# Optimization experiments

Hardware: AMD Instinct MI355X
Metric: run time of the kernel (lower is better)

Reference implementation:

```python
import jax, jax.numpy as jnp
import numpy as np

H = 512      # hidden_channels
NP = 20000   # politician nodes
NS = 10000   # stock nodes
E = 400000   # edges per relation / trade edges
FP = 64      # raw politician feature dim
FS = 64      # raw stock feature dim
NC = 3       # num_classes


def setup_inputs() -> dict:
    key = jax.random.key(0)
    ks = iter(jax.random.split(key, 40))

    def rn(shape, s=0.05):
        return (jax.random.normal(next(ks), shape, jnp.float32) * s).astype(jnp.float32)

    inp = {}
    inp["x_pol"] = rn((NP, FP), 1.0)
    inp["x_stock"] = rn((NS, FS), 1.0)
    inp["trade_edge_attr"] = rn((E, 2), 1.0)
    # input projections (torch Linear: y = x @ W + b)
    inp["Wp"] = rn((FP, H)); inp["bp"] = rn((H,))
    inp["Ws"] = rn((FS, H)); inp["bs"] = rn((H,))
    # SAGEConv params: Wl/bl act on mean-aggregated neighbors, Wr on root (no bias)
    for layer in ("c1", "c2"):
        for rel in ("ps", "sp"):
            inp[f"{layer}_{rel}_Wl"] = rn((H, H))
            inp[f"{layer}_{rel}_bl"] = rn((H,))
            inp[f"{layer}_{rel}_Wr"] = rn((H, H))
    # decoder MLP
    inp["d1_W"] = rn((2 * H + 2, H)); inp["d1_b"] = rn((H,))
    inp["d2_W"] = rn((H, NC)); inp["d2_b"] = rn((NC,))
    # edge indices
    inp["edge_ps_src"] = jax.random.randint(next(ks), (E,), 0, NP, jnp.int64 if jax.config.jax_enable_x64 else jnp.int32)
    inp["edge_ps_dst"] = jax.random.randint(next(ks), (E,), 0, NS, jnp.int32)
    inp["edge_sp_src"] = jax.random.randint(next(ks), (E,), 0, NS, jnp.int32)
    inp["edge_sp_dst"] = jax.random.randint(next(ks), (E,), 0, NP, jnp.int32)
    inp["trade_row"] = jax.random.randint(next(ks), (E,), 0, NP, jnp.int32)
    inp["trade_col"] = jax.random.randint(next(ks), (E,), 0, NS, jnp.int32)
    inp["edge_ps_src"] = inp["edge_ps_src"].astype(jnp.int32)
    return inp


def sage_conv(x_src, x_dst, src, dst, Wl, bl, Wr, n_dst):
    # PyG SAGEConv (aggr='mean', root_weight=True, normalize=False):
    # out = lin_l(mean_{j->i} x_j) + lin_r(x_i)
    msg = x_src[src]                                            # [E, H] gather
    agg = jax.ops.segment_sum(msg, dst, num_segments=n_dst)     # [n_dst, H]
    cnt = jax.ops.segment_sum(jnp.ones((src.shape[0], 1), x_src.dtype), dst, num_segments=n_dst)
    mean = agg / jnp.maximum(cnt, 1.0)
    return mean @ Wl + bl + x_dst @ Wr


def reference(x_pol, x_stock, trade_edge_attr,
              Wp, bp, Ws, bs,
              c1_ps_Wl, c1_ps_bl, c1_ps_Wr, c1_sp_Wl, c1_sp_bl, c1_sp_Wr,
              c2_ps_Wl, c2_ps_bl, c2_ps_Wr, c2_sp_Wl, c2_sp_bl, c2_sp_Wr,
              d1_W, d1_b, d2_W, d2_b,
              edge_ps_src, edge_ps_dst, edge_sp_src, edge_sp_dst,
              trade_row, trade_col):
    # per-node-type input projection + relu
    hp = jax.nn.relu(x_pol @ Wp + bp)      # [NP, H]
    hs = jax.nn.relu(x_stock @ Ws + bs)    # [NS, H]
    # conv1 (HeteroConv sum: each node type is dst of exactly one relation)
    hs1 = sage_conv(hp, hs, edge_ps_src, edge_ps_dst, c1_ps_Wl, c1_ps_bl, c1_ps_Wr, hs.shape[0])
    hp1 = sage_conv(hs, hp, edge_sp_src, edge_sp_dst, c1_sp_Wl, c1_sp_bl, c1_sp_Wr, hp.shape[0])
    hp1, hs1 = jax.nn.relu(hp1), jax.nn.relu(hs1)
    # conv2
    hs2 = sage_conv(hp1, hs1, edge_ps_src, edge_ps_dst, c2_ps_Wl, c2_ps_bl, c2_ps_Wr, hs1.shape[0])
    hp2 = sage_conv(hs1, hp1, edge_sp_src, edge_sp_dst, c2_sp_Wl, c2_sp_bl, c2_sp_Wr, hp1.shape[0])
    hp2, hs2 = jax.nn.relu(hp2), jax.nn.relu(hs2)
    # edge decoder (Dropout is identity at inference)
    feat = jnp.concatenate([hp2[trade_row], hs2[trade_col], trade_edge_attr], axis=-1)  # [E, 2H+2]
    h = jax.nn.relu(feat @ d1_W + d1_b)
    return h @ d2_W + d2_b  # [E, NC]
```

## Files before the change

kernel.cpp:

```cpp
#include <hip/hip_runtime.h>
#include <hip/hip_bf16.h>

typedef unsigned short u16;
typedef unsigned int u32;
typedef __attribute__((ext_vector_type(8))) short short8;
typedef __attribute__((ext_vector_type(4))) float f32x4;

#define NP 20000
#define NS 10000
#define NE 400000
#define H  512
#define FDIM 64
#define ECHUNK 16

__device__ __forceinline__ float bl16(u32 w){ return __uint_as_float(w << 16); }
__device__ __forceinline__ float bh16(u32 w){ return __uint_as_float(w & 0xffff0000u); }
__device__ __forceinline__ u16 f2bf(float f){
  u32 u = __float_as_uint(f);
  u32 r = u + 0x7fffu + ((u >> 16) & 1u);
  return (u16)(r >> 16);
}
__device__ __forceinline__ u32 pack2(float a, float b){
  return (u32)f2bf(a) | ((u32)f2bf(b) << 16);
}
__device__ __forceinline__ void gload16(const void* g, void* l){
  __builtin_amdgcn_global_load_lds((const __attribute__((address_space(1))) u32*)g,
                                   (__attribute__((address_space(3))) u32*)l, 16, 0, 0);
}

__global__ __launch_bounds__(256) void proj_kernel(const float* __restrict__ X, const float* __restrict__ W,
                                                   const float* __restrict__ b, u16* __restrict__ Y, int n)
{
  __shared__ float xs[8][FDIM];
  int tid = threadIdx.x;
  int m0 = blockIdx.x * 8;
  {
    int r = tid >> 6, c = tid & 63;
    int m = m0 + r;
    xs[r][c] = (m < n) ? X[(size_t)m*FDIM + c] : 0.f;
    m = m0 + r + 4;
    xs[r+4][c] = (m < n) ? X[(size_t)m*FDIM + c] : 0.f;
  }
  __syncthreads();
  float acc[8][2] = {};
  int c0 = tid, c1 = tid + 256;
  for (int k = 0; k < FDIM; ++k){
    float w0 = W[k*H + c0];
    float w1 = W[k*H + c1];
    #pragma unroll
    for (int r = 0; r < 8; ++r){
      float xv = xs[r][k];
      acc[r][0] = fmaf(xv, w0, acc[r][0]);
      acc[r][1] = fmaf(xv, w1, acc[r][1]);
    }
  }
  float b0 = b[c0], b1 = b[c1];
  #pragma unroll
  for (int r = 0; r < 8; ++r){
    int m = m0 + r;
    if (m < n){
      Y[(size_t)m*H + c0] = f2bf(fmaxf(acc[r][0] + b0, 0.f));
      Y[(size_t)m*H + c1] = f2bf(fmaxf(acc[r][1] + b1, 0.f));
    }
  }
}

struct TPair { const float* src; u16* dst; };
struct TArgs { TPair m[10]; };

__global__ __launch_bounds__(256) void wtrans_kernel(TArgs args)
{
  __shared__ float lds[32][33];
  int mat = blockIdx.z;
  const float* __restrict__ src = args.m[mat].src;
  u16* __restrict__ dst = args.m[mat].dst;
  int k0 = blockIdx.y << 5, n0 = blockIdx.x << 5;
  int t = threadIdx.x;
  int r = t >> 3, c4 = (t & 7) << 2;
  float4 v = *(const float4*)(src + (size_t)(k0 + r)*H + n0 + c4);
  lds[r][c4+0] = v.x; lds[r][c4+1] = v.y; lds[r][c4+2] = v.z; lds[r][c4+3] = v.w;
  __syncthreads();
  uint2 o;
  o.x = pack2(lds[c4+0][r], lds[c4+1][r]);
  o.y = pack2(lds[c4+2][r], lds[c4+3][r]);
  *(uint2*)(dst + (size_t)(n0 + r)*H + k0 + c4) = o;
}

__global__ void hist_kernel(const int* __restrict__ ps_dst, const int* __restrict__ sp_dst,
                            const int* __restrict__ trow,
                            int* __restrict__ cnt_s, int* __restrict__ cnt_p, int* __restrict__ cnt_t)
{
  int e = blockIdx.x * blockDim.x + threadIdx.x;
  if (e < NE){
    atomicAdd(&cnt_s[ps_dst[e]], 1);
    atomicAdd(&cnt_p[sp_dst[e]], 1);
    atomicAdd(&cnt_t[trow[e]], 1);
  }
}

__device__ void scan_one(int* cnt, int n, int* rowptr)
{
  __shared__ int lds[1024];
  __shared__ int carry_s;
  int tid = threadIdx.x;
  if (tid == 0) carry_s = 0;
  __syncthreads();
  for (int base = 0; base < n; base += 1024){
    int i = base + tid;
    int v = (i < n) ? cnt[i] : 0;
    lds[tid] = v;
    __syncthreads();
    for (int off = 1; off < 1024; off <<= 1){
      int t = (tid >= off) ? lds[tid - off] : 0;
      __syncthreads();
      lds[tid] += t;
      __syncthreads();
    }
    int incl = lds[tid];
    int cb = carry_s;
    if (i < n){
      rowptr[i] = cb + incl - v;
      cnt[i] = cb + incl - v;
    }
    __syncthreads();
    if (tid == 0) carry_s = cb + lds[1023];
    __syncthreads();
  }
  if (tid == 0) rowptr[n] = carry_s;
}

__global__ __launch_bounds__(1024) void scan3_kernel(int* c0, int n0, int* r0,
                                                     int* c1, int n1, int* r1,
                                                     int* c2, int n2, int* r2)
{
  if (blockIdx.x == 0) scan_one(c0, n0, r0);
  else if (blockIdx.x == 1) scan_one(c1, n1, r1);
  else scan_one(c2, n2, r2);
}

__global__ void scatter_kernel(const int* __restrict__ ps_src, const int* __restrict__ ps_dst,
                               const int* __restrict__ sp_src, const int* __restrict__ sp_dst,
                               const int* __restrict__ trow, const int* __restrict__ tcol,
                               const float* __restrict__ attr,
                               int* __restrict__ cur_s, int* __restrict__ cur_p, int* __restrict__ cur_t,
                               int* __restrict__ sorted_ps, int* __restrict__ sorted_sp,
                               int4* __restrict__ meta_t, float2* __restrict__ attr_t)
{
  int e = blockIdx.x * blockDim.x + threadIdx.x;
  if (e < NE){
    int pos = atomicAdd(&cur_s[ps_dst[e]], 1);
    sorted_ps[pos] = ps_src[e];
    int pos2 = atomicAdd(&cur_p[sp_dst[e]], 1);
    sorted_sp[pos2] = sp_src[e];
    int r = trow[e];
    int pos3 = atomicAdd(&cur_t[r], 1);
    meta_t[pos3] = make_int4(e, r, tcol[e], 0);
    attr_t[pos3] = make_float2(attr[2*e], attr[2*e+1]);
  }
}

__global__ __launch_bounds__(256) void agg2_kernel(
    const u16* __restrict__ X0, const int* __restrict__ rp0, const int* __restrict__ s0,
    u16* __restrict__ M0, int n0,
    const u16* __restrict__ X1, const int* __restrict__ rp1, const int* __restrict__ s1,
    u16* __restrict__ M1, int n1)
{
  int wid = (blockIdx.x << 2) + (threadIdx.x >> 6);
  int lane = threadIdx.x & 63;
  const u16* X; const int* rp; const int* ss; u16* M; int row;
  if (wid < n0){ X = X0; rp = rp0; ss = s0; M = M0; row = wid; }
  else if (wid < n0 + n1){ X = X1; rp = rp1; ss = s1; M = M1; row = wid - n0; }
  else return;
  int beg = rp[row], end = rp[row + 1];
  float acc[8] = {0,0,0,0,0,0,0,0};
  int j0 = lane << 3;
#define ACCV(v) { acc[0] += bl16(v.x); acc[1] += bh16(v.x); \
                  acc[2] += bl16(v.y); acc[3] += bh16(v.y); \
                  acc[4] += bl16(v.z); acc[5] += bh16(v.z); \
                  acc[6] += bl16(v.w); acc[7] += bh16(v.w); }
  int i = beg;
  for (; i + 4 <= end; i += 4){
    int sa = ss[i], sb = ss[i+1], sc = ss[i+2], sd = ss[i+3];
    uint4 v0 = *(const uint4*)(X + (size_t)sa*H + j0);
    uint4 v1 = *(const uint4*)(X + (size_t)sb*H + j0);
    uint4 v2 = *(const uint4*)(X + (size_t)sc*H + j0);
    uint4 v3 = *(const uint4*)(X + (size_t)sd*H + j0);
    ACCV(v0); ACCV(v1); ACCV(v2); ACCV(v3);
  }
  for (; i < end; ++i){
    int sa = ss[i];
    uint4 v0 = *(const uint4*)(X + (size_t)sa*H + j0);
    ACCV(v0);
  }
#undef ACCV
  float inv = 1.f / (float)max(end - beg, 1);
  uint4 o;
  o.x = pack2(acc[0]*inv, acc[1]*inv);
  o.y = pack2(acc[2]*inv, acc[3]*inv);
  o.z = pack2(acc[4]*inv, acc[5]*inv);
  o.w = pack2(acc[6]*inv, acc[7]*inv);
  *(uint4*)(M + (size_t)row*H + j0) = o;
}

struct GemmProb {
  const u16* A1; const u16* W1t; const u16* A2; const u16* W2t;
  const float* bias; u16* C; int nrows; int relu;
};

__global__ __launch_bounds__(256) void gemm_mfma2(GemmProb Pa, GemmProb Pb)
{
  GemmProb P = blockIdx.z ? Pb : Pa;
  int m0 = blockIdx.y << 7, n0 = blockIdx.x << 7;
  if (m0 >= P.nrows) return;

  __shared__ u16 As[128*64];
  __shared__ u16 Bs[128*64];
  char* AsB = (char*)As;
  char* BsB = (char*)Bs;
  int t = threadIdx.x;
  int w = t >> 6, l = t & 63;
  int wr = w >> 1, wc = w & 1;
  int lr = l & 15, lg = l >> 4;

  f32x4 acc[4][4];
  #pragma unroll
  for (int i = 0; i < 4; ++i)
    #pragma unroll
    for (int j = 0; j < 4; ++j)
      acc[i][j] = (f32x4){0.f, 0.f, 0.f, 0.f};

  for (int phase = 0; phase < 2; ++phase){
    const u16* Ap = phase ? P.A2 : P.A1;
    const u16* Wp = phase ? P.W2t : P.W1t;
    if (!Ap) break;
    for (int k0 = 0; k0 < H; k0 += 64){
      #pragma unroll
      for (int i = 0; i < 4; ++i){
        int c = i*256 + t;
        int row = c >> 3, p = c & 7;
        int k8 = p ^ (row & 7);
        gload16(Ap + (size_t)(m0 + row)*H + k0 + k8*8, AsB + c*16);
        gload16(Wp + (size_t)(n0 + row)*H + k0 + k8*8, BsB + c*16);
      }
      __syncthreads();
      #pragma unroll
      for (int ks = 0; ks < 2; ++ks){
        short8 a[4], b[4];
        int kc = (ks << 2) + lg;
        #pragma unroll
        for (int mi = 0; mi < 4; ++mi){
          int r = (wr << 6) + (mi << 4) + lr;
          a[mi] = *(const short8*)(AsB + r*128 + ((kc ^ (r & 7)) << 4));
        }
        #pragma unroll
        for (int ni = 0; ni < 4; ++ni){
          int r = (wc << 6) + (ni << 4) + lr;
          b[ni] = *(const short8*)(BsB + r*128 + ((kc ^ (r & 7)) << 4));
        }
        #pragma unroll
        for (int mi = 0; mi < 4; ++mi)
          #pragma unroll
          for (int ni = 0; ni < 4; ++ni)
            acc[mi][ni] = __builtin_amdgcn_mfma_f32_16x16x32_bf16(a[mi], b[ni], acc[mi][ni], 0, 0, 0);
      }
      __syncthreads();
    }
  }

  float bv[4];
  #pragma unroll
  for (int ni = 0; ni < 4; ++ni)
    bv[ni] = P.bias ? P.bias[n0 + (wc << 6) + (ni << 4) + lr] : 0.f;
  #pragma unroll
  for (int mi = 0; mi < 4; ++mi){
    #pragma unroll
    for (int j = 0; j < 4; ++j){
      int m = m0 + (wr << 6) + (mi << 4) + (lg << 2) + j;
      if (m < P.nrows){
        #pragma unroll
        for (int ni = 0; ni < 4; ++ni){
          float v = acc[mi][ni][j] + bv[ni];
          if (P.relu) v = fmaxf(v, 0.f);
          P.C[(size_t)m*H + n0 + (wc << 6) + (ni << 4) + lr] = f2bf(v);
        }
      }
    }
  }
}

__global__ __launch_bounds__(256) void edge_chunk_kernel(
    const u16* __restrict__ Adec, const u16* __restrict__ Bdec,
    const float* __restrict__ d1W, const float* __restrict__ d1b,
    const float* __restrict__ d2W, const float* __restrict__ d2b,
    const int4* __restrict__ meta_t, const float2* __restrict__ attr_t,
    float* __restrict__ out)
{
  int lane = threadIdx.x & 63;
  int ch = (blockIdx.x << 2) + (threadIdx.x >> 6);
  int base = ch * ECHUNK;
  if (base >= NE) return;
  int j0 = lane << 3;

  float w1a[8], w1b[8], bb[8], w2[8][3];
  #pragma unroll
  for (int q = 0; q < 8; ++q){
    w1a[q] = d1W[(size_t)1024*H + j0 + q];
    w1b[q] = d1W[(size_t)1025*H + j0 + q];
    bb[q]  = d1b[j0 + q];
    w2[q][0] = d2W[(j0+q)*3 + 0];
    w2[q][1] = d2W[(j0+q)*3 + 1];
    w2[q][2] = d2W[(j0+q)*3 + 2];
  }
  float ob0 = d2b[0], ob1 = d2b[1], ob2 = d2b[2];

  int cached_r = -1;
  float fa[8];

  auto compute = [&](int e, float a0, float a1, uint4 vb){
    float fb[8] = {bl16(vb.x),bh16(vb.x),bl16(vb.y),bh16(vb.y),
                   bl16(vb.z),bh16(vb.z),bl16(vb.w),bh16(vb.w)};
    float s0 = 0.f, s1 = 0.f, s2 = 0.f;
    #pragma unroll
    for (int q = 0; q < 8; ++q){
      float h = fa[q] + fb[q];
      h = fmaf(a0, w1a[q], h);
      h = fmaf(a1, w1b[q], h);
      h = fmaxf(h, 0.f);
      s0 = fmaf(h, w2[q][0], s0);
      s1 = fmaf(h, w2[q][1], s1);
      s2 = fmaf(h, w2[q][2], s2);
    }
    #pragma unroll
    for (int off = 32; off > 0; off >>= 1){
      s0 += __shfl_xor(s0, off);
      s1 += __shfl_xor(s1, off);
      s2 += __shfl_xor(s2, off);
    }
    if (lane == 0){
      out[(size_t)e*3 + 0] = s0 + ob0;
      out[(size_t)e*3 + 1] = s1 + ob1;
      out[(size_t)e*3 + 2] = s2 + ob2;
    }
  };
  auto loadA = [&](int r){
    cached_r = r;
    uint4 va = *(const uint4*)(Adec + (size_t)r*H + j0);
    fa[0] = bl16(va.x)+bb[0]; fa[1] = bh16(va.x)+bb[1];
    fa[2] = bl16(va.y)+bb[2]; fa[3] = bh16(va.y)+bb[3];
    fa[4] = bl16(va.z)+bb[4]; fa[5] = bh16(va.z)+bb[5];
    fa[6] = bl16(va.w)+bb[6]; fa[7] = bh16(va.w)+bb[7];
  };

  int4 mA = meta_t[base + 0];
  int4 mB = meta_t[base + 1];
  float2 aA = attr_t[base + 0];
  float2 aB = attr_t[base + 1];
  uint4 vbA = *(const uint4*)(Bdec + (size_t)mA.z*H + j0);
  uint4 vbB = *(const uint4*)(Bdec + (size_t)mB.z*H + j0);

  for (int i = 0; i < ECHUNK; i += 2){
    int4 mA2 = {}, mB2 = {};
    float2 aA2 = {}, aB2 = {};
    uint4 vbA2 = {}, vbB2 = {};
    if (i + 2 < ECHUNK){
      mA2 = meta_t[base + i + 2];
      mB2 = meta_t[base + i + 3];
      aA2 = attr_t[base + i + 2];
      aB2 = attr_t[base + i + 3];
      vbA2 = *(const uint4*)(Bdec + (size_t)mA2.z*H + j0);
      vbB2 = *(const uint4*)(Bdec + (size_t)mB2.z*H + j0);
    }
    if (mA.y != cached_r) loadA(mA.y);
    compute(mA.x, aA.x, aA.y, vbA);
    if (mB.y != cached_r) loadA(mB.y);
    compute(mB.x, aB.x, aB.y, vbB);
    mA = mA2; mB = mB2; aA = aA2; aB = aB2; vbA = vbA2; vbB = vbB2;
  }
}

extern "C" void kernel_launch(void* const* d_in, const int* in_sizes, int n_in,
                              void* d_out, int out_size, void* d_ws, size_t ws_size,
                              hipStream_t stream)
{
  const float* x_pol    = (const float*)d_in[0];
  const float* x_stock  = (const float*)d_in[1];
  const float* attr     = (const float*)d_in[2];
  const float* Wp       = (const float*)d_in[3];
  const float* bp       = (const float*)d_in[4];
  const float* Wst      = (const float*)d_in[5];
  const float* bst      = (const float*)d_in[6];
  const float* c1_ps_Wl = (const float*)d_in[7];
  const float* c1_ps_bl = (const float*)d_in[8];
  const float* c1_ps_Wr = (const float*)d_in[9];
  const float* c1_sp_Wl = (const float*)d_in[10];
  const float* c1_sp_bl = (const float*)d_in[11];
  const float* c1_sp_Wr = (const float*)d_in[12];
  const float* c2_ps_Wl = (const float*)d_in[13];
  const float* c2_ps_bl = (const float*)d_in[14];
  const float* c2_ps_Wr = (const float*)d_in[15];
  const float* c2_sp_Wl = (const float*)d_in[16];
  const float* c2_sp_bl = (const float*)d_in[17];
  const float* c2_sp_Wr = (const float*)d_in[18];
  const float* d1W      = (const float*)d_in[19];
  const float* d1b      = (const float*)d_in[20];
  const float* d2W      = (const float*)d_in[21];
  const float* d2b      = (const float*)d_in[22];
  const int* ps_src     = (const int*)d_in[23];
  const int* ps_dst     = (const int*)d_in[24];
  const int* sp_src     = (const int*)d_in[25];
  const int* sp_dst     = (const int*)d_in[26];
  const int* trow       = (const int*)d_in[27];
  const int* tcol       = (const int*)d_in[28];
  float* out = (float*)d_out;

  char* ws = (char*)d_ws;
  size_t off = 0;
  auto alloc = [&](size_t bytes)->char*{
    char* p = ws + off;
    off += (bytes + 255) & ~(size_t)255;
    return p;
  };
  u16* P0 = (u16*)alloc((size_t)NP*H*2);
  u16* P1 = (u16*)alloc((size_t)NP*H*2);
  u16* S0 = (u16*)alloc((size_t)NS*H*2);
  u16* S1 = (u16*)alloc((size_t)NS*H*2);
  u16* MP = (u16*)alloc((size_t)NP*H*2);
  u16* MS = (u16*)alloc((size_t)NS*H*2);
  u16* Wt[10];
  for (int i = 0; i < 10; ++i) Wt[i] = (u16*)alloc((size_t)H*H*2);
  int* cnt_s    = (int*)alloc((size_t)NS*4);
  int* cnt_p    = (int*)alloc((size_t)NP*4);
  int* cnt_t    = (int*)alloc((size_t)NP*4);
  int* rowptr_s = (int*)alloc((size_t)(NS+1)*4);
  int* rowptr_p = (int*)alloc((size_t)(NP+1)*4);
  int* rowptr_t = (int*)alloc((size_t)(NP+1)*4);
  int* sorted_ps = (int*)alloc((size_t)NE*4);
  int* sorted_sp = (int*)alloc((size_t)NE*4);
  int4* meta_t   = (int4*)alloc((size_t)NE*16);
  float2* attr_t = (float2*)alloc((size_t)NE*8);
  alloc((size_t)128*H*2);

  TArgs ta;
  ta.m[0] = {c1_ps_Wl, Wt[0]}; ta.m[1] = {c1_ps_Wr, Wt[1]};
  ta.m[2] = {c1_sp_Wl, Wt[2]}; ta.m[3] = {c1_sp_Wr, Wt[3]};
  ta.m[4] = {c2_ps_Wl, Wt[4]}; ta.m[5] = {c2_ps_Wr, Wt[5]};
  ta.m[6] = {c2_sp_Wl, Wt[6]}; ta.m[7] = {c2_sp_Wr, Wt[7]};
  ta.m[8] = {d1W, Wt[8]};
  ta.m[9] = {d1W + (size_t)512*H, Wt[9]};
  wtrans_kernel<<<dim3(16,16,10), 256, 0, stream>>>(ta);

  hipMemsetAsync(cnt_s, 0, (size_t)NS*4, stream);
  hipMemsetAsync(cnt_p, 0, (size_t)NP*4, stream);
  hipMemsetAsync(cnt_t, 0, (size_t)NP*4, stream);
  hist_kernel<<<(NE+255)/256, 256, 0, stream>>>(ps_dst, sp_dst, trow, cnt_s, cnt_p, cnt_t);
  scan3_kernel<<<3, 1024, 0, stream>>>(cnt_s, NS, rowptr_s, cnt_p, NP, rowptr_p, cnt_t, NP, rowptr_t);
  scatter_kernel<<<(NE+255)/256, 256, 0, stream>>>(ps_src, ps_dst, sp_src, sp_dst, trow, tcol, attr,
                                                   cnt_s, cnt_p, cnt_t,
                                                   sorted_ps, sorted_sp, meta_t, attr_t);

  proj_kernel<<<(NP+7)/8, 256, 0, stream>>>(x_pol, Wp, bp, P0, NP);
  proj_kernel<<<(NS+7)/8, 256, 0, stream>>>(x_stock, Wst, bst, S0, NS);

  int aggGrid = (NS + NP + 3) / 4;
  int gRows = (NP + 127) / 128;

  agg2_kernel<<<aggGrid, 256, 0, stream>>>(P0, rowptr_s, sorted_ps, MS, NS,
                                           S0, rowptr_p, sorted_sp, MP, NP);
  {
    GemmProb a = {MS, Wt[0], S0, Wt[1], c1_ps_bl, S1, NS, 1};
    GemmProb b = {MP, Wt[2], P0, Wt[3], c1_sp_bl, P1, NP, 1};
    gemm_mfma2<<<dim3(4, gRows, 2), 256, 0, stream>>>(a, b);
  }

  agg2_kernel<<<aggGrid, 256, 0, stream>>>(P1, rowptr_s, sorted_ps, MS, NS,
                                           S1, rowptr_p, sorted_sp, MP, NP);
  {
    GemmProb a = {MS, Wt[4], S1, Wt[5], c2_ps_bl, S0, NS, 1};
    GemmProb b = {MP, Wt[6], P1, Wt[7], c2_sp_bl, P0, NP, 1};
    gemm_mfma2<<<dim3(4, gRows, 2), 256, 0, stream>>>(a, b);
  }

  {
    GemmProb a = {P0, Wt[8], nullptr, nullptr, nullptr, MP, NP, 0};
    GemmProb b = {S0, Wt[9], nullptr, nullptr, nullptr, MS, NS, 0};
    gemm_mfma2<<<dim3(4, gRows, 2), 256, 0, stream>>>(a, b);
  }

  int nchunks = NE / ECHUNK;
  edge_chunk_kernel<<<(nchunks + 3) / 4, 256, 0, stream>>>(MP, MS, d1W, d1b, d2W, d2b,
                                                           meta_t, attr_t, out);
}
```

Before: 657.9 us.

## Use packed FP32 math, wave-shuffle scan, deeper gather unroll and lane-distributed edge metadata

Three kernels change at once. The scan kernel replaces its barrier-heavy LDS Hillis-Steele scan with a two-level wavefront shuffle scan. The aggregation kernel unrolls the neighbor gather to 8 loads in flight and accumulates with v_pk_add_f32. The edge decoder loads a chunk's edge metadata once per lane, broadcasts it with shuffles, keeps a 4-deep prefetch ring of B rows, and does the MLP math with packed FP32 FMA. The aim is fewer barriers, more memory-level parallelism and fewer VALU instructions, at the cost of more registers and inline asm that may constrain scheduling.

```diff
diff --git a/kernel.cpp b/kernel.cpp
--- a/kernel.cpp
+++ b/kernel.cpp
@@ -5,6 +5,7 @@
 typedef unsigned int u32;
 typedef __attribute__((ext_vector_type(8))) short short8;
 typedef __attribute__((ext_vector_type(4))) float f32x4;
+typedef __attribute__((ext_vector_type(2))) float f32x2;
 
 #define NP 20000
 #define NS 10000
@@ -26,6 +27,16 @@
 __device__ __forceinline__ void gload16(const void* g, void* l){
   __builtin_amdgcn_global_load_lds((const __attribute__((address_space(1))) u32*)g,
                                    (__attribute__((address_space(3))) u32*)l, 16, 0, 0);
+}
+__device__ __forceinline__ f32x2 pk_fma(f32x2 a, f32x2 b, f32x2 c){
+  f32x2 d;
+  asm("v_pk_fma_f32 %0, %1, %2, %3" : "=v"(d) : "v"(a), "v"(b), "v"(c));
+  return d;
+}
+__device__ __forceinline__ f32x2 pk_add(f32x2 a, f32x2 b){
+  f32x2 d;
+  asm("v_pk_add_f32 %0, %1, %2" : "=v"(d) : "v"(a), "v"(b));
+  return d;
 }
 
 __global__ __launch_bounds__(256) void proj_kernel(const float* __restrict__ X, const float* __restrict__ W,
@@ -100,32 +111,41 @@
 
 __device__ void scan_one(int* cnt, int n, int* rowptr)
 {
-  __shared__ int lds[1024];
+  __shared__ int wsum[16];
   __shared__ int carry_s;
   int tid = threadIdx.x;
+  int lane = tid & 63, wv = tid >> 6;
   if (tid == 0) carry_s = 0;
-  __syncthreads();
   for (int base = 0; base < n; base += 1024){
+    __syncthreads();
     int i = base + tid;
     int v = (i < n) ? cnt[i] : 0;
-    lds[tid] = v;
+    int x = v;
+    #pragma unroll
+    for (int off = 1; off < 64; off <<= 1){
+      int t = __shfl_up(x, off);
+      if (lane >= off) x += t;
+    }
+    if (lane == 63) wsum[wv] = x;
     __syncthreads();
-    for (int off = 1; off < 1024; off <<= 1){
-      int t = (tid >= off) ? lds[tid - off] : 0;
-      __syncthreads();
-      lds[tid] += t;
-      __syncthreads();
-    }
-    int incl = lds[tid];
+    if (wv == 0 && lane < 16){
+      int y = wsum[lane];
+      #pragma unroll
+      for (int off = 1; off < 16; off <<= 1){
+        int t = __shfl_up(y, off, 16);
+        if (lane >= off) y += t;
+      }
+      wsum[lane] = y;
+    }
+    __syncthreads();
+    int woff = (wv > 0) ? wsum[wv-1] : 0;
     int cb = carry_s;
-    if (i < n){
-      rowptr[i] = cb + incl - v;
-      cnt[i] = cb + incl - v;
-    }
+    int excl = cb + woff + x - v;
+    if (i < n){ rowptr[i] = excl; cnt[i] = excl; }
     __syncthreads();
-    if (tid == 0) carry_s = cb + lds[1023];
-    __syncthreads();
-  }
+    if (tid == 1023) carry_s = cb + woff + x;
+  }
+  __syncthreads();
   if (tid == 0) rowptr[n] = carry_s;
 }
 
@@ -172,33 +192,45 @@
   else if (wid < n0 + n1){ X = X1; rp = rp1; ss = s1; M = M1; row = wid - n0; }
   else return;
   int beg = rp[row], end = rp[row + 1];
-  float acc[8] = {0,0,0,0,0,0,0,0};
+  f32x2 ac0 = {0,0}, ac1 = {0,0}, ac2 = {0,0}, ac3 = {0,0};
   int j0 = lane << 3;
-#define ACCV(v) { acc[0] += bl16(v.x); acc[1] += bh16(v.x); \
-                  acc[2] += bl16(v.y); acc[3] += bh16(v.y); \
-                  acc[4] += bl16(v.z); acc[5] += bh16(v.z); \
-                  acc[6] += bl16(v.w); acc[7] += bh16(v.w); }
+#define ACCP(v) { ac0 = pk_add(ac0, (f32x2){bl16(v.x), bh16(v.x)}); \
+                  ac1 = pk_add(ac1, (f32x2){bl16(v.y), bh16(v.y)}); \
+                  ac2 = pk_add(ac2, (f32x2){bl16(v.z), bh16(v.z)}); \
+                  ac3 = pk_add(ac3, (f32x2){bl16(v.w), bh16(v.w)}); }
   int i = beg;
-  for (; i + 4 <= end; i += 4){
-    int sa = ss[i], sb = ss[i+1], sc = ss[i+2], sd = ss[i+3];
+  for (; i + 8 <= end; i += 8){
+    int sa = ss[i+0], sb = ss[i+1], sc = ss[i+2], sd = ss[i+3];
+    int se = ss[i+4], sf = ss[i+5], sg = ss[i+6], sh = ss[i+7];
     uint4 v0 = *(const uint4*)(X + (size_t)sa*H + j0);
     uint4 v1 = *(const uint4*)(X + (size_t)sb*H + j0);
     uint4 v2 = *(const uint4*)(X + (size_t)sc*H + j0);
     uint4 v3 = *(const uint4*)(X + (size_t)sd*H + j0);
-    ACCV(v0); ACCV(v1); ACCV(v2); ACCV(v3);
-  }
-  for (; i < end; ++i){
+    uint4 v4 = *(const uint4*)(X + (size_t)se*H + j0);
+    uint4 v5 = *(const uint4*)(X + (size_t)sf*H + j0);
+    uint4 v6 = *(const uint4*)(X + (size_t)sg*H + j0);
+    uint4 v7 = *(const uint4*)(X + (size_t)sh*H + j0);
+    ACCP(v0); ACCP(v1); ACCP(v2); ACCP(v3);
+    ACCP(v4); ACCP(v5); ACCP(v6); ACCP(v7);
+  }
+  for (; i + 2 <= end; i += 2){
+    int sa = ss[i], sb = ss[i+1];
+    uint4 v0 = *(const uint4*)(X + (size_t)sa*H + j0);
+    uint4 v1 = *(const uint4*)(X + (size_t)sb*H + j0);
+    ACCP(v0); ACCP(v1);
+  }
+  if (i < end){
     int sa = ss[i];
     uint4 v0 = *(const uint4*)(X + (size_t)sa*H + j0);
-    ACCV(v0);
-  }
-#undef ACCV
+    ACCP(v0);
+  }
+#undef ACCP
   float inv = 1.f / (float)max(end - beg, 1);
   uint4 o;
-  o.x = pack2(acc[0]*inv, acc[1]*inv);
-  o.y = pack2(acc[2]*inv, acc[3]*inv);
-  o.z = pack2(acc[4]*inv, acc[5]*inv);
-  o.w = pack2(acc[6]*inv, acc[7]*inv);
+  o.x = pack2(ac0.x*inv, ac0.y*inv);
+  o.y = pack2(ac1.x*inv, ac1.y*inv);
+  o.z = pack2(ac2.x*inv, ac2.y*inv);
+  o.w = pack2(ac3.x*inv, ac3.y*inv);
   *(uint4*)(M + (size_t)row*H + j0) = o;
 }
 
@@ -301,80 +333,80 @@
   if (base >= NE) return;
   int j0 = lane << 3;
 
-  float w1a[8], w1b[8], bb[8], w2[8][3];
-  #pragma unroll
-  for (int q = 0; q < 8; ++q){
-    w1a[q] = d1W[(size_t)1024*H + j0 + q];
-    w1b[q] = d1W[(size_t)1025*H + j0 + q];
-    bb[q]  = d1b[j0 + q];
-    w2[q][0] = d2W[(j0+q)*3 + 0];
-    w2[q][1] = d2W[(j0+q)*3 + 1];
-    w2[q][2] = d2W[(j0+q)*3 + 2];
+  f32x2 w1a2[4], w1b2[4], bb2[4], w20[4], w21[4], w22[4];
+  #pragma unroll
+  for (int q = 0; q < 4; ++q){
+    int c = j0 + 2*q;
+    w1a2[q] = (f32x2){ d1W[(size_t)1024*H + c], d1W[(size_t)1024*H + c + 1] };
+    w1b2[q] = (f32x2){ d1W[(size_t)1025*H + c], d1W[(size_t)1025*H + c + 1] };
+    bb2[q]  = (f32x2){ d1b[c], d1b[c+1] };
+    w20[q]  = (f32x2){ d2W[c*3 + 0], d2W[(c+1)*3 + 0] };
+    w21[q]  = (f32x2){ d2W[c*3 + 1], d2W[(c+1)*3 + 1] };
+    w22[q]  = (f32x2){ d2W[c*3 + 2], d2W[(c+1)*3 + 2] };
   }
   float ob0 = d2b[0], ob1 = d2b[1], ob2 = d2b[2];
 
+  int4 mv = make_int4(0,0,0,0);
+  float2 av = make_float2(0.f,0.f);
+  if (lane < ECHUNK){ mv = meta_t[base + lane]; av = attr_t[base + lane]; }
+
   int cached_r = -1;
-  float fa[8];
-
-  auto compute = [&](int e, float a0, float a1, uint4 vb){
-    float fb[8] = {bl16(vb.x),bh16(vb.x),bl16(vb.y),bh16(vb.y),
-                   bl16(vb.z),bh16(vb.z),bl16(vb.w),bh16(vb.w)};
-    float s0 = 0.f, s1 = 0.f, s2 = 0.f;
-    #pragma unroll
-    for (int q = 0; q < 8; ++q){
-      float h = fa[q] + fb[q];
-      h = fmaf(a0, w1a[q], h);
-      h = fmaf(a1, w1b[q], h);
-      h = fmaxf(h, 0.f);
-      s0 = fmaf(h, w2[q][0], s0);
-      s1 = fmaf(h, w2[q][1], s1);
-      s2 = fmaf(h, w2[q][2], s2);
-    }
-    #pragma unroll
-    for (int off = 32; off > 0; off >>= 1){
-      s0 += __shfl_xor(s0, off);
-      s1 += __shfl_xor(s1, off);
-      s2 += __shfl_xor(s2, off);
-    }
-    if (lane == 0){
-      out[(size_t)e*3 + 0] = s0 + ob0;
-      out[(size_t)e*3 + 1] = s1 + ob1;
-      out[(size_t)e*3 + 2] = s2 + ob2;
-    }
-  };
+  f32x2 fa2[4];
   auto loadA = [&](int r){
     cached_r = r;
     uint4 va = *(const uint4*)(Adec + (size_t)r*H + j0);
-    fa[0] = bl16(va.x)+bb[0]; fa[1] = bh16(va.x)+bb[1];
-    fa[2] = bl16(va.y)+bb[2]; fa[3] = bh16(va.y)+bb[3];
-    fa[4] = bl16(va.z)+bb[4]; fa[5] = bh16(va.z)+bb[5];
-    fa[6] = bl16(va.w)+bb[6]; fa[7] = bh16(va.w)+bb[7];
+    fa2[0] = pk_add((f32x2){bl16(va.x), bh16(va.x)}, bb2[0]);
+    fa2[1] = pk_add((f32x2){bl16(va.y), bh16(va.y)}, bb2[1]);
+    fa2[2] = pk_add((f32x2){bl16(va.z), bh16(va.z)}, bb2[2]);
+    fa2[3] = pk_add((f32x2){bl16(va.w), bh16(va.w)}, bb2[3]);
   };
 
-  int4 mA = meta_t[base + 0];
-  int4 mB = meta_t[base + 1];
-  float2 aA = attr_t[base + 0];
-  float2 aB = attr_t[base + 1];
-  uint4 vbA = *(const uint4*)(Bdec + (size_t)mA.z*H + j0);
-  uint4 vbB = *(const uint4*)(Bdec + (size_t)mB.z*H + j0);
-
-  for (int i = 0; i < ECHUNK; i += 2){
-    int4 mA2 = {}, mB2 = {};
-    float2 aA2 = {}, aB2 = {};
-    uint4 vbA2 = {}, vbB2 = {};
-    if (i + 2 < ECHUNK){
-      mA2 = meta_t[base + i + 2];
-      mB2 = meta_t[base + i + 3];
-      aA2 = attr_t[base + i + 2];
-      aB2 = attr_t[base + i + 3];
-      vbA2 = *(const uint4*)(Bdec + (size_t)mA2.z*H + j0);
-      vbB2 = *(const uint4*)(Bdec + (size_t)mB2.z*H + j0);
-    }
-    if (mA.y != cached_r) loadA(mA.y);
-    compute(mA.x, aA.x, aA.y, vbA);
-    if (mB.y != cached_r) loadA(mB.y);
-    compute(mB.x, aB.x, aB.y, vbB);
-    mA = mA2; mB = mB2; aA = aA2; aB = aB2; vbA = vbA2; vbB = vbB2;
+  uint4 vb[4];
+  #pragma unroll
+  for (int d = 0; d < 4; ++d){
+    int c = __shfl(mv.z, d);
+    vb[d] = *(const uint4*)(Bdec + (size_t)c*H + j0);
+  }
+
+  #pragma unroll
+  for (int i = 0; i < ECHUNK; ++i){
+    uint4 vc = vb[i & 3];
+    if (i + 4 < ECHUNK){
+      int cn = __shfl(mv.z, i + 4);
+      vb[i & 3] = *(const uint4*)(Bdec + (size_t)cn*H + j0);
+    }
+    int e  = __shfl(mv.x, i);
+    int r  = __shfl(mv.y, i);
+    float a0 = __shfl(av.x, i);
+    float a1 = __shfl(av.y, i);
+    if (r != cached_r) loadA(r);
+
+    f32x2 a0v = (f32x2){a0, a0}, a1v = (f32x2){a1, a1};
+    f32x2 fb[4] = { (f32x2){bl16(vc.x), bh16(vc.x)}, (f32x2){bl16(vc.y), bh16(vc.y)},
+                    (f32x2){bl16(vc.z), bh16(vc.z)}, (f32x2){bl16(vc.w), bh16(vc.w)} };
+    f32x2 s0 = {0,0}, s1 = {0,0}, s2 = {0,0};
+    #pragma unroll
+    for (int q = 0; q < 4; ++q){
+      f32x2 u = pk_add(fa2[q], fb[q]);
+      u = pk_fma(a0v, w1a2[q], u);
+      u = pk_fma(a1v, w1b2[q], u);
+      u.x = fmaxf(u.x, 0.f); u.y = fmaxf(u.y, 0.f);
+      s0 = pk_fma(u, w20[q], s0);
+      s1 = pk_fma(u, w21[q], s1);
+      s2 = pk_fma(u, w22[q], s2);
+    }
+    float r0 = s0.x + s0.y, r1 = s1.x + s1.y, r2 = s2.x + s2.y;
+    #pragma unroll
+    for (int off = 32; off > 0; off >>= 1){
+      r0 += __shfl_xor(r0, off);
+      r1 += __shfl_xor(r1, off);
+      r2 += __shfl_xor(r2, off);
+    }
+    if (lane == 0){
+      out[(size_t)e*3 + 0] = r0 + ob0;
+      out[(size_t)e*3 + 1] = r1 + ob1;
+      out[(size_t)e*3 + 2] = r2 + ob2;
+    }
   }
 }
 
```

After: 628.4 us. -4.5%, faster.
